# Optimization experiments

Hardware: AMD Instinct MI355X
Metric: run time of the kernel (lower is better)

The kernel has to match this reference:

```python
import jax, jax.numpy as jnp
import numpy as np

N, E, G = 50000, 400000, 64
IN_C, HID, OUT_C, HEADS = 256, 128, 256, 4
LRELU_SLOPE = 0.2
LN_EPS = 1e-5


def setup_inputs() -> dict:
    key = jax.random.key(0)
    ks = jax.random.split(key, 16)
    d = {}
    d["x"] = jax.random.normal(ks[0], (N, IN_C), dtype=jnp.float32)
    d["edge_index"] = jax.random.randint(ks[1], (2, E), 0, N, dtype=jnp.int32)
    d["batch"] = jnp.sort(jax.random.randint(ks[2], (N,), 0, G, dtype=jnp.int32))
    s1 = 1.0 / np.sqrt(IN_C)
    d["W1"] = jax.random.uniform(ks[3], (IN_C, HEADS * HID), jnp.float32, -s1, s1)
    d["att_src1"] = jax.random.normal(ks[4], (HEADS, HID), jnp.float32) * 0.1
    d["att_dst1"] = jax.random.normal(ks[5], (HEADS, HID), jnp.float32) * 0.1
    d["b1"] = jnp.zeros((HEADS * HID,), jnp.float32)
    d["ln1_g"] = jnp.ones((HEADS * HID,), jnp.float32)
    d["ln1_b"] = jnp.zeros((HEADS * HID,), jnp.float32)
    s2 = 1.0 / np.sqrt(HEADS * HID)
    d["W2"] = jax.random.uniform(ks[6], (HEADS * HID, OUT_C), jnp.float32, -s2, s2)
    d["att_src2"] = jax.random.normal(ks[7], (1, OUT_C), jnp.float32) * 0.1
    d["att_dst2"] = jax.random.normal(ks[8], (1, OUT_C), jnp.float32) * 0.1
    d["b2"] = jnp.zeros((OUT_C,), jnp.float32)
    d["ln2_g"] = jnp.ones((OUT_C,), jnp.float32)
    d["ln2_b"] = jnp.zeros((OUT_C,), jnp.float32)
    return d


def _layernorm(x, g, b):
    mu = jnp.mean(x, axis=-1, keepdims=True)
    var = jnp.mean(jnp.square(x - mu), axis=-1, keepdims=True)
    return (x - mu) * jax.lax.rsqrt(var + LN_EPS) * g + b


def _gat_conv(x, src, dst, W, a_src, a_dst, bias):
    # PyG GATConv (eval mode, dropout inactive), self-loops already in src/dst.
    H, C = a_src.shape
    h = (x @ W).reshape(N, H, C)                       # [N,H,C]
    e_src = jnp.einsum('nhc,hc->nh', h, a_src)          # [N,H]
    e_dst = jnp.einsum('nhc,hc->nh', h, a_dst)
    e = jax.nn.leaky_relu(e_src[src] + e_dst[dst], LRELU_SLOPE)  # [Etot,H]
    m = jax.ops.segment_max(e, dst, num_segments=N)     # segment softmax over incoming edges
    ex = jnp.exp(e - m[dst])
    s = jax.ops.segment_sum(ex, dst, num_segments=N)
    alpha = ex / (s[dst] + 1e-16)                       # [Etot,H]
    msg = h[src] * alpha[:, :, None]                    # [Etot,H,C]
    out = jax.ops.segment_sum(msg, dst, num_segments=N) # [N,H,C]
    return out.reshape(N, H * C) + bias


def reference(x, edge_index, batch, W1, att_src1, att_dst1, b1, ln1_g, ln1_b,
              W2, att_src2, att_dst2, b2, ln2_g, ln2_b):
    loops = jnp.arange(N, dtype=edge_index.dtype)
    src = jnp.concatenate([edge_index[0], loops])
    dst = jnp.concatenate([edge_index[1], loops])
    h = _gat_conv(x, src, dst, W1, att_src1, att_dst1, b1)
    h = _layernorm(h, ln1_g, ln1_b)
    h = jax.nn.relu(h)                                  # dropout is identity in eval
    h = _gat_conv(h, src, dst, W2, att_src2, att_dst2, b2)
    h = _layernorm(h, ln2_g, ln2_b)
    # global_mean_pool over graphs
    sums = jax.ops.segment_sum(h, batch, num_segments=G)
    cnts = jax.ops.segment_sum(jnp.ones((N,), h.dtype), batch, num_segments=G)
    return sums / jnp.maximum(cnts, 1.0)[:, None]
```

## Files before the change

kernel.cpp:

```cpp
#include <hip/hip_runtime.h>
#include <hip/hip_bf16.h>
#include <cstdint>

#define LRELU_SLOPE 0.2f

typedef short bf16x8 __attribute__((ext_vector_type(8)));
typedef float f32x4  __attribute__((ext_vector_type(4)));

__device__ __forceinline__ float b2f(unsigned short u) {
  return __uint_as_float(((unsigned int)u) << 16);
}
__device__ __forceinline__ unsigned short f2b(float f) {
  unsigned int u = __float_as_uint(f);
  return (unsigned short)((u + 0x7fff + ((u >> 16) & 1)) >> 16);
}

__device__ __forceinline__ void gload16(const void* g, void* l) {
  __builtin_amdgcn_global_load_lds(
      (const __attribute__((address_space(1))) unsigned int*)g,
      (__attribute__((address_space(3))) unsigned int*)l, 16, 0, 0);
}

__global__ __launch_bounds__(256)
void prep_x_count(const float* __restrict__ x, unsigned short* __restrict__ o,
                  int M, int Mpad, const int* __restrict__ ei, int E, int Etot,
                  int* __restrict__ count) {
  const int i = blockIdx.x * 256 + threadIdx.x;
  if (i < Mpad * 64) {
    const int row = i >> 6;
    const int c4  = (i & 63) * 4;
    ushort4 v = make_ushort4(0, 0, 0, 0);
    if (row < M) {
      const float4 f = *(const float4*)&x[(size_t)row * 256 + c4];
      v = make_ushort4(f2b(f.x), f2b(f.y), f2b(f.z), f2b(f.w));
    }
    *(ushort4*)&o[(size_t)row * 256 + c4] = v;
  }
  if (i < Etot) {
    const int d = (i < E) ? ei[E + i] : (i - E);
    atomicAdd(&count[d], 1);
  }
}

__global__ __launch_bounds__(256)
void cvt_wts(const float* __restrict__ W1, const float* __restrict__ W2,
             unsigned short* __restrict__ W1T, unsigned short* __restrict__ W2T) {
  int j = blockIdx.x * 256 + threadIdx.x;
  if (j < 512 * 256) {
    const int n = j >> 8, k = j & 255;
    W1T[j] = f2b(W1[(size_t)k * 512 + n]);
  } else {
    j -= 512 * 256;
    const int n = j >> 9, k = j & 511;
    W2T[j] = f2b(W2[(size_t)k * 256 + n]);
  }
}

__global__ __launch_bounds__(256)
void scan_blocksum(const int* __restrict__ count, int* __restrict__ bsum, int Nn) {
  const int i0 = blockIdx.x * 1024 + threadIdx.x * 4;
  int s = 0;
#pragma unroll
  for (int k = 0; k < 4; ++k) { const int i = i0 + k; if (i < Nn) s += count[i]; }
#pragma unroll
  for (int off = 1; off < 64; off <<= 1) s += __shfl_xor(s, off);
  __shared__ int ws[4];
  if ((threadIdx.x & 63) == 0) ws[threadIdx.x >> 6] = s;
  __syncthreads();
  if (threadIdx.x == 0) bsum[blockIdx.x] = ws[0] + ws[1] + ws[2] + ws[3];
}

__global__ __launch_bounds__(64)
void scan_top(const int* __restrict__ bsum, int* __restrict__ boff,
              int* __restrict__ rowptrN, int nb) {
  const int t = threadIdx.x;
  const int v = (t < nb) ? bsum[t] : 0;
  int incl = v;
#pragma unroll
  for (int off = 1; off < 64; off <<= 1) {
    const int u = __shfl_up(incl, off);
    if (t >= off) incl += u;
  }
  if (t < nb) boff[t] = incl - v;
  if (t == 63) *rowptrN = incl;
}

__global__ __launch_bounds__(256)
void scan_apply(const int* __restrict__ count, const int* __restrict__ boff,
                int* __restrict__ rowptr, int* __restrict__ cursor, int Nn) {
  const int t = threadIdx.x;
  const int lane = t & 63;
  const int w = t >> 6;
  const int i0 = blockIdx.x * 1024 + t * 4;
  int c[4]; int s = 0;
#pragma unroll
  for (int k = 0; k < 4; ++k) { const int i = i0 + k; c[k] = (i < Nn) ? count[i] : 0; s += c[k]; }
  int incl = s;
#pragma unroll
  for (int off = 1; off < 64; off <<= 1) {
    const int u = __shfl_up(incl, off);
    if (lane >= off) incl += u;
  }
  __shared__ int ws[4];
  if (lane == 63) ws[w] = incl;
  __syncthreads();
  int woff = 0;
  for (int k = 0; k < w; ++k) woff += ws[k];
  int base = boff[blockIdx.x] + woff + incl - s;
#pragma unroll
  for (int k = 0; k < 4; ++k) {
    const int i = i0 + k;
    if (i < Nn) { rowptr[i] = base; cursor[i] = base; base += c[k]; }
  }
}

__global__ __launch_bounds__(256)
void csr_scatter(const int* __restrict__ ei, int E, int Etot,
                 int* __restrict__ cursor, int* __restrict__ srcs,
                 int* __restrict__ dsts) {
  const int i = blockIdx.x * 256 + threadIdx.x;
  if (i >= Etot) return;
  const int s = (i < E) ? ei[i]     : (i - E);
  const int d = (i < E) ? ei[E + i] : (i - E);
  const int pos = atomicAdd(&cursor[d], 1);
  srcs[pos] = s;
  dsts[pos] = d;
}

template<int KSTEPS>
__global__ __launch_bounds__(256)
void gemm_bf16(const unsigned short* __restrict__ A,
               const unsigned short* __restrict__ BT,
               unsigned short* __restrict__ C, int M, int Nn, int K,
               const float* __restrict__ asrc, const float* __restrict__ adst,
               float* __restrict__ es, float* __restrict__ ed,
               int H, int lgC, int esPart) {
  __shared__ __align__(16) unsigned short smA[2][64 * 32];
  __shared__ __align__(16) unsigned short smB[2][128 * 32];
  const int tid  = threadIdx.x;
  const int lane = tid & 63;
  const int wid  = tid >> 6;
  const int wm = wid >> 1, wn = wid & 1;
  const int brow = blockIdx.y * 64;
  const int bcol = blockIdx.x * 128;
  const int u = lane >> 4, r15 = lane & 15;
  const int arow = tid >> 2, aslot = tid & 3;
  const size_t aBase = (size_t)(brow + arow) * K + (aslot ^ (arow & 3)) * 8;
  const int ldsA = arow * 32 + aslot * 8;
  const int brow0 = tid >> 2,        bslot0 = tid & 3;
  const int brow1 = (256 + tid) >> 2, bslot1 = tid & 3;
  const size_t bBase0 = (size_t)(bcol + brow0) * K + (bslot0 ^ (brow0 & 3)) * 8;
  const size_t bBase1 = (size_t)(bcol + brow1) * K + (bslot1 ^ (brow1 & 3)) * 8;
  const int ldsB0 = brow0 * 32 + bslot0 * 8;
  const int ldsB1 = brow1 * 32 + bslot1 * 8;

  auto stage = [&](int buf, int ks) {
    const int k0 = ks * 32;
    gload16(A + aBase + k0, &smA[buf][ldsA]);
    gload16(BT + bBase0 + k0, &smB[buf][ldsB0]);
    gload16(BT + bBase1 + k0, &smB[buf][ldsB1]);
  };

  f32x4 acc[2][4] = {};
  const int sw = u ^ (r15 & 3);

  stage(0, 0);
  asm volatile("s_waitcnt vmcnt(0)" ::: "memory");
  __syncthreads();
  int cur = 0;
#pragma unroll
  for (int ks = 0; ks < KSTEPS; ++ks) {
    if (ks + 1 < KSTEPS) stage(cur ^ 1, ks + 1);
    bf16x8 af[2], bfv[4];
#pragma unroll
    for (int m = 0; m < 2; ++m) {
      const int row = wm * 32 + m * 16 + r15;
      af[m] = *(const bf16x8*)&smA[cur][row * 32 + sw * 8];
    }
#pragma unroll
    for (int n = 0; n < 4; ++n) {
      const int col = wn * 64 + n * 16 + r15;
      bfv[n] = *(const bf16x8*)&smB[cur][col * 32 + sw * 8];
    }
#pragma unroll
    for (int m = 0; m < 2; ++m)
#pragma unroll
      for (int n = 0; n < 4; ++n)
        acc[m][n] = __builtin_amdgcn_mfma_f32_16x16x32_bf16(
            af[m], bfv[n], acc[m][n], 0, 0, 0);
    if (ks + 1 < KSTEPS) {
      asm volatile("s_waitcnt vmcnt(0)" ::: "memory");
      __syncthreads();
      cur ^= 1;
    }
  }

  __syncthreads();
  unsigned short* cb = &smB[0][0];
#pragma unroll
  for (int m = 0; m < 2; ++m)
#pragma unroll
    for (int n = 0; n < 4; ++n) {
      const int col = wn * 64 + n * 16 + r15;
#pragma unroll
      for (int rr = 0; rr < 4; ++rr) {
        const int row = wm * 32 + m * 16 + u * 4 + rr;
        cb[row * 128 + col] = f2b(acc[m][n][rr]);
      }
    }
  __syncthreads();
#pragma unroll
  for (int i = 0; i < 4; ++i) {
    const int idx = (i * 256 + tid) * 8;
    const int row = idx >> 7;
    const int cc  = idx & 127;
    const int grow = brow + row;
    if (grow < M)
      *(float4*)&C[(size_t)grow * Nn + bcol + cc] = *(const float4*)&cb[idx];
  }

  es += (size_t)blockIdx.x * esPart;
  ed += (size_t)blockIdx.x * esPart;
  const int head = bcol >> lgC;
  float asv[4], adv[4];
#pragma unroll
  for (int n = 0; n < 4; ++n) {
    const int cc = bcol + wn * 64 + n * 16 + r15;
    asv[n] = asrc[cc];
    adv[n] = adst[cc];
  }
#pragma unroll
  for (int m = 0; m < 2; ++m) {
#pragma unroll
    for (int rr = 0; rr < 4; ++rr) {
      float pes = 0.f, ped = 0.f;
#pragma unroll
      for (int n = 0; n < 4; ++n) {
        pes = fmaf(acc[m][n][rr], asv[n], pes);
        ped = fmaf(acc[m][n][rr], adv[n], ped);
      }
#pragma unroll
      for (int off = 1; off < 16; off <<= 1) {
        pes += __shfl_xor(pes, off);
        ped += __shfl_xor(ped, off);
      }
      if (r15 == 0) {
        const int row = brow + wm * 32 + m * 16 + u * 4 + rr;
        if (row < M) {
          unsafeAtomicAdd(&es[row * H + head], pes);
          unsafeAtomicAdd(&ed[row * H + head], ped);
        }
      }
    }
  }
}

template<int H>
__global__ __launch_bounds__(256)
void ex_compute(const int* __restrict__ srcs, const int* __restrict__ dsts,
                const float* __restrict__ es, const float* __restrict__ ed,
                float* __restrict__ exCSR, int Etot, int pN) {
  const int p = blockIdx.x * 256 + threadIdx.x;
  if (p >= Etot) return;
  const int sN = srcs[p], dN = dsts[p];
  if constexpr (H == 4) {
    const float4 a = *(const float4*)&es[sN * 4];
    const float4 b = *(const float4*)&ed[dN * 4];
    float e0 = a.x + b.x, e1 = a.y + b.y, e2 = a.z + b.z, e3 = a.w + b.w;
    e0 = (e0 > 0.f) ? e0 : LRELU_SLOPE * e0;
    e1 = (e1 > 0.f) ? e1 : LRELU_SLOPE * e1;
    e2 = (e2 > 0.f) ? e2 : LRELU_SLOPE * e2;
    e3 = (e3 > 0.f) ? e3 : LRELU_SLOPE * e3;
    *(float4*)&exCSR[p * 4] =
        make_float4(__expf(e0), __expf(e1), __expf(e2), __expf(e3));
  } else {
    float e = (es[sN] + es[pN + sN]) + (ed[dN] + ed[pN + dN]);
    e = (e > 0.f) ? e : LRELU_SLOPE * e;
    exCSR[p] = __expf(e);
  }
}

template<int H, int C, bool RELU, bool BFOUT>
__global__ __launch_bounds__(256)
void gat_agg_ln(const int* __restrict__ rowptr, const int* __restrict__ srcs,
                const float* __restrict__ exCSR,
                const unsigned short* __restrict__ h,
                const float* __restrict__ bias, const float* __restrict__ lng,
                const float* __restrict__ lnb, unsigned short* __restrict__ obf,
                float* __restrict__ of32, int Nn) {
  constexpr int HC = H * C;
  constexpr int F  = HC / 64;
  const int wave = threadIdx.x >> 6;
  const int lane = threadIdx.x & 63;
  const int n = blockIdx.x * 4 + wave;
  if (n >= Nn) return;
  const int beg = rowptr[n];
  const int deg = rowptr[n + 1] - beg;
  const int hl = (lane * F) / C;

  float dsum = 0.f;
  if constexpr (H == 4) {
    for (int it = lane; it < deg * 4; it += 64) dsum += exCSR[beg * 4 + it];
#pragma unroll
    for (int off = 4; off < 64; off <<= 1) dsum += __shfl_xor(dsum, off);
    dsum = __shfl(dsum, hl);
  } else {
    for (int it = lane; it < deg; it += 64) dsum += exCSR[beg + it];
#pragma unroll
    for (int off = 1; off < 64; off <<= 1) dsum += __shfl_xor(dsum, off);
  }
  const float inv_s = 1.0f / (dsum + 1e-16f);

  float acc[F];
#pragma unroll
  for (int i = 0; i < F; ++i) acc[i] = 0.f;

  auto fma_rows = [&](const ushort4* v0, const ushort4* v1, const float* a, int cnt) {
    for (int q = 0; q < cnt; ++q) {
      acc[0] = fmaf(b2f(v0[q].x), a[q], acc[0]);
      acc[1] = fmaf(b2f(v0[q].y), a[q], acc[1]);
      acc[2] = fmaf(b2f(v0[q].z), a[q], acc[2]);
      acc[3] = fmaf(b2f(v0[q].w), a[q], acc[3]);
      if constexpr (F == 8) {
        acc[4] = fmaf(b2f(v1[q].x), a[q], acc[4]);
        acc[5] = fmaf(b2f(v1[q].y), a[q], acc[5]);
        acc[6] = fmaf(b2f(v1[q].z), a[q], acc[6]);
        acc[7] = fmaf(b2f(v1[q].w), a[q], acc[7]);
      }
    }
  };

  int j = 0;
  for (; j + 4 <= deg; j += 4) {
    int s4[4];
    float a4[4];
#pragma unroll
    for (int q = 0; q < 4; ++q) s4[q] = srcs[beg + j + q];
#pragma unroll
    for (int q = 0; q < 4; ++q) a4[q] = exCSR[(beg + j + q) * H + hl] * inv_s;
    ushort4 v0[4], v1[4];
#pragma unroll
    for (int q = 0; q < 4; ++q) {
      const unsigned short* hp = &h[(size_t)s4[q] * HC + lane * F];
      v0[q] = *(const ushort4*)hp;
      if constexpr (F == 8) v1[q] = *(const ushort4*)(hp + 4);
    }
    fma_rows(v0, v1, a4, 4);
  }
  for (; j < deg; ++j) {
    const int src = srcs[beg + j];
    const float a = exCSR[(beg + j) * H + hl] * inv_s;
    const unsigned short* hp = &h[(size_t)src * HC + lane * F];
    ushort4 v0 = *(const ushort4*)hp, v1;
    if constexpr (F == 8) v1 = *(const ushort4*)(hp + 4);
    fma_rows(&v0, &v1, &a, 1);
  }

#pragma unroll
  for (int i = 0; i < F; i += 4) {
    const float4 bb = *(const float4*)&bias[lane * F + i];
    acc[i + 0] += bb.x; acc[i + 1] += bb.y;
    acc[i + 2] += bb.z; acc[i + 3] += bb.w;
  }
  float sum = 0.f, sq = 0.f;
#pragma unroll
  for (int i = 0; i < F; ++i) { sum += acc[i]; sq += acc[i] * acc[i]; }
#pragma unroll
  for (int off = 1; off < 64; off <<= 1) {
    sum += __shfl_xor(sum, off);
    sq  += __shfl_xor(sq, off);
  }
  const float mu  = sum / HC;
  const float var = sq / HC - mu * mu;
  const float r   = rsqrtf(var + 1e-5f);
  float y[F];
#pragma unroll
  for (int i = 0; i < F; i += 4) {
    const float4 gg = *(const float4*)&lng[lane * F + i];
    const float4 bl = *(const float4*)&lnb[lane * F + i];
    y[i + 0] = (acc[i + 0] - mu) * r * gg.x + bl.x;
    y[i + 1] = (acc[i + 1] - mu) * r * gg.y + bl.y;
    y[i + 2] = (acc[i + 2] - mu) * r * gg.z + bl.z;
    y[i + 3] = (acc[i + 3] - mu) * r * gg.w + bl.w;
  }
  if constexpr (RELU) {
#pragma unroll
    for (int i = 0; i < F; ++i) y[i] = fmaxf(y[i], 0.f);
  }
  if constexpr (BFOUT) {
    unsigned short* op = &obf[(size_t)n * HC + lane * F];
    *(ushort4*)op = make_ushort4(f2b(y[0]), f2b(y[1]), f2b(y[2]), f2b(y[3]));
    if constexpr (F == 8)
      *(ushort4*)(op + 4) = make_ushort4(f2b(y[4]), f2b(y[5]), f2b(y[6]), f2b(y[7]));
  } else {
    float* op = &of32[(size_t)n * HC + lane * F];
    *(float4*)op = make_float4(y[0], y[1], y[2], y[3]);
    if constexpr (F == 8)
      *(float4*)(op + 4) = make_float4(y[4], y[5], y[6], y[7]);
  }
}

__global__ __launch_bounds__(256)
void pool_partial(const unsigned short* __restrict__ x, const int* __restrict__ batch,
                  float* __restrict__ tmp, int* __restrict__ cnt, int Nn) {
  const int r0 = blockIdx.x * 64;
  const int rend = min(r0 + 64, Nn);
  const int t = threadIdx.x;
  float acc = 0.f;
  int cur = batch[r0];
  int seglen = 0;
  for (int r = r0; r < rend; ++r) {
    const int g = batch[r];
    if (g != cur) {
      unsafeAtomicAdd(&tmp[cur * 256 + t], acc);
      if (t == 0) atomicAdd(&cnt[cur], seglen);
      acc = 0.f; seglen = 0; cur = g;
    }
    acc += b2f(x[(size_t)r * 256 + t]);
    ++seglen;
  }
  unsafeAtomicAdd(&tmp[cur * 256 + t], acc);
  if (t == 0) atomicAdd(&cnt[cur], seglen);
}

__global__ __launch_bounds__(256)
void pool_final(const float* __restrict__ tmp, const int* __restrict__ cnt,
                float* __restrict__ out) {
  const int g = blockIdx.x;
  const int t = threadIdx.x;
  out[g * 256 + t] = tmp[g * 256 + t] / fmaxf((float)cnt[g], 1.f);
}

extern "C" void kernel_launch(void* const* d_in, const int* in_sizes, int n_in,
                              void* d_out, int out_size, void* d_ws, size_t ws_size,
                              hipStream_t stream) {
  const float* x    = (const float*)d_in[0];
  const int*   ei   = (const int*)d_in[1];
  const int*   batch= (const int*)d_in[2];
  const float* W1   = (const float*)d_in[3];
  const float* as1  = (const float*)d_in[4];
  const float* ad1  = (const float*)d_in[5];
  const float* b1   = (const float*)d_in[6];
  const float* g1   = (const float*)d_in[7];
  const float* be1  = (const float*)d_in[8];
  const float* W2   = (const float*)d_in[9];
  const float* as2  = (const float*)d_in[10];
  const float* ad2  = (const float*)d_in[11];
  const float* b2   = (const float*)d_in[12];
  const float* g2   = (const float*)d_in[13];
  const float* be2  = (const float*)d_in[14];

  const int N    = in_sizes[0] / 256;
  const int E    = in_sizes[1] / 2;
  const int Etot = E + N;
  const int Mpad = ((N + 63) / 64) * 64;
  const int NB   = (N + 1023) / 1024;

  float* ws = (float*)d_ws;
  unsigned short* out2 = (unsigned short*)ws;
  unsigned short* A2bf = out2 + (size_t)N * 256;
  unsigned short* A1bf = A2bf;
  unsigned short* h1bf = A2bf + (size_t)Mpad * 512;
  unsigned short* W1T  = h1bf + (size_t)N * 512;
  unsigned short* W2T  = W1T + 512 * 256;
  float* es1 = (float*)(W2T + 512 * 256);
  float* ed1 = es1 + (size_t)N * 4;
  float* es2 = ed1 + (size_t)N * 4;
  float* ed2 = es2 + (size_t)N * 2;
  int* count  = (int*)(ed2 + (size_t)N * 2);
  int* rowptr = count + N;
  int* cursor = rowptr + N + 4;
  int* srcs   = cursor + N;
  int* dsts   = srcs + Etot;
  float* exCSR = (float*)(dsts + Etot);
  float* ptmp = exCSR + (size_t)Etot * 4;
  int*   pcnt = (int*)(ptmp + 64 * 256);
  int*   bsum = pcnt + 64;
  int*   boff = bsum + 64;
  unsigned short* h2bf = h1bf;

  const int eb = (Etot + 255) / 256;

  hipMemsetAsync(es1, 0, (size_t)N * 13 * 4, stream);
  hipMemsetAsync(ptmp, 0, (size_t)(64 * 256 + 64) * 4, stream);
  hipMemsetAsync(A2bf + (size_t)N * 512, 0, (size_t)(Mpad - N) * 512 * 2, stream);

  prep_x_count<<<(Mpad * 64 + 255) / 256, 256, 0, stream>>>(
      x, A1bf, N, Mpad, ei, E, Etot, count);
  cvt_wts<<<(2 * 512 * 256 + 255) / 256, 256, 0, stream>>>(W1, W2, W1T, W2T);

  scan_blocksum<<<NB, 256, 0, stream>>>(count, bsum, N);
  scan_top<<<1, 64, 0, stream>>>(bsum, boff, &rowptr[N], NB);
  scan_apply<<<NB, 256, 0, stream>>>(count, boff, rowptr, cursor, N);
  csr_scatter<<<eb, 256, 0, stream>>>(ei, E, Etot, cursor, srcs, dsts);

  gemm_bf16<8><<<dim3(4, Mpad / 64), 256, 0, stream>>>(
      A1bf, W1T, h1bf, N, 512, 256, as1, ad1, es1, ed1, 4, 7, 0);
  ex_compute<4><<<eb, 256, 0, stream>>>(srcs, dsts, es1, ed1, exCSR, Etot, 0);
  gat_agg_ln<4, 128, true, true><<<(N + 3) / 4, 256, 0, stream>>>(
      rowptr, srcs, exCSR, h1bf, b1, g1, be1, A2bf, nullptr, N);

  gemm_bf16<16><<<dim3(2, Mpad / 64), 256, 0, stream>>>(
      A2bf, W2T, h2bf, N, 256, 512, as2, ad2, es2, ed2, 1, 8, N);
  ex_compute<1><<<eb, 256, 0, stream>>>(srcs, dsts, es2, ed2, exCSR, Etot, N);
  gat_agg_ln<1, 256, false, true><<<(N + 3) / 4, 256, 0, stream>>>(
      rowptr, srcs, exCSR, h2bf, b2, g2, be2, out2, nullptr, N);

  pool_partial<<<(N + 63) / 64, 256, 0, stream>>>(out2, batch, ptmp, pcnt, N);
  pool_final<<<64, 256, 0, stream>>>(ptmp, pcnt, (float*)d_out);
}
```

Before: 319.2 us.

## Shrink GEMM N-tile to 64, unroll aggregation by 8 with packed bf16 loads

The GEMM block tile goes from 64x128 to 64x64, which doubles the grid and halves LDS and accumulator usage. Layer 2 therefore splits its attention-score partials across four column blocks, and both the es/ed buffers and the memset grow to match. The aggregation kernel now gathers 8 neighbor rows at a time using wide uint4/uint2 loads and unpacks bf16 pairs with bit ops, to expose more memory-level parallelism. The smaller tile reloads the A operand more often and adds more atomic adds for the attention scores.

```diff
diff --git a/kernel.cpp b/kernel.cpp
--- a/kernel.cpp
+++ b/kernel.cpp
@@ -135,33 +135,27 @@
                const float* __restrict__ asrc, const float* __restrict__ adst,
                float* __restrict__ es, float* __restrict__ ed,
                int H, int lgC, int esPart) {
-  __shared__ __align__(16) unsigned short smA[2][64 * 32];
-  __shared__ __align__(16) unsigned short smB[2][128 * 32];
+  __shared__ __align__(16) unsigned short sm[2][4096];
   const int tid  = threadIdx.x;
   const int lane = tid & 63;
   const int wid  = tid >> 6;
   const int wm = wid >> 1, wn = wid & 1;
   const int brow = blockIdx.y * 64;
-  const int bcol = blockIdx.x * 128;
+  const int bcol = blockIdx.x * 64;
   const int u = lane >> 4, r15 = lane & 15;
-  const int arow = tid >> 2, aslot = tid & 3;
-  const size_t aBase = (size_t)(brow + arow) * K + (aslot ^ (arow & 3)) * 8;
-  const int ldsA = arow * 32 + aslot * 8;
-  const int brow0 = tid >> 2,        bslot0 = tid & 3;
-  const int brow1 = (256 + tid) >> 2, bslot1 = tid & 3;
-  const size_t bBase0 = (size_t)(bcol + brow0) * K + (bslot0 ^ (brow0 & 3)) * 8;
-  const size_t bBase1 = (size_t)(bcol + brow1) * K + (bslot1 ^ (brow1 & 3)) * 8;
-  const int ldsB0 = brow0 * 32 + bslot0 * 8;
-  const int ldsB1 = brow1 * 32 + bslot1 * 8;
+  const int srow = tid >> 2, sslot = tid & 3;
+  const int sswz = sslot ^ (srow & 3);
+  const size_t aBase = (size_t)(brow + srow) * K + sswz * 8;
+  const size_t bBase = (size_t)(bcol + srow) * K + sswz * 8;
+  const int ldsOff = srow * 32 + sslot * 8;
 
   auto stage = [&](int buf, int ks) {
     const int k0 = ks * 32;
-    gload16(A + aBase + k0, &smA[buf][ldsA]);
-    gload16(BT + bBase0 + k0, &smB[buf][ldsB0]);
-    gload16(BT + bBase1 + k0, &smB[buf][ldsB1]);
+    gload16(A + aBase + k0, &sm[buf][ldsOff]);
+    gload16(BT + bBase + k0, &sm[buf][2048 + ldsOff]);
   };
 
-  f32x4 acc[2][4] = {};
+  f32x4 acc[2][2] = {};
   const int sw = u ^ (r15 & 3);
 
   stage(0, 0);
@@ -171,21 +165,21 @@
 #pragma unroll
   for (int ks = 0; ks < KSTEPS; ++ks) {
     if (ks + 1 < KSTEPS) stage(cur ^ 1, ks + 1);
-    bf16x8 af[2], bfv[4];
+    bf16x8 af[2], bfv[2];
 #pragma unroll
     for (int m = 0; m < 2; ++m) {
       const int row = wm * 32 + m * 16 + r15;
-      af[m] = *(const bf16x8*)&smA[cur][row * 32 + sw * 8];
-    }
-#pragma unroll
-    for (int n = 0; n < 4; ++n) {
-      const int col = wn * 64 + n * 16 + r15;
-      bfv[n] = *(const bf16x8*)&smB[cur][col * 32 + sw * 8];
+      af[m] = *(const bf16x8*)&sm[cur][row * 32 + sw * 8];
+    }
+#pragma unroll
+    for (int n = 0; n < 2; ++n) {
+      const int col = wn * 32 + n * 16 + r15;
+      bfv[n] = *(const bf16x8*)&sm[cur][2048 + col * 32 + sw * 8];
     }
 #pragma unroll
     for (int m = 0; m < 2; ++m)
 #pragma unroll
-      for (int n = 0; n < 4; ++n)
+      for (int n = 0; n < 2; ++n)
         acc[m][n] = __builtin_amdgcn_mfma_f32_16x16x32_bf16(
             af[m], bfv[n], acc[m][n], 0, 0, 0);
     if (ks + 1 < KSTEPS) {
@@ -196,24 +190,24 @@
   }
 
   __syncthreads();
-  unsigned short* cb = &smB[0][0];
+  unsigned short* cb = &sm[0][0];
 #pragma unroll
   for (int m = 0; m < 2; ++m)
 #pragma unroll
-    for (int n = 0; n < 4; ++n) {
-      const int col = wn * 64 + n * 16 + r15;
+    for (int n = 0; n < 2; ++n) {
+      const int col = wn * 32 + n * 16 + r15;
 #pragma unroll
       for (int rr = 0; rr < 4; ++rr) {
         const int row = wm * 32 + m * 16 + u * 4 + rr;
-        cb[row * 128 + col] = f2b(acc[m][n][rr]);
+        cb[row * 64 + col] = f2b(acc[m][n][rr]);
       }
     }
   __syncthreads();
 #pragma unroll
-  for (int i = 0; i < 4; ++i) {
+  for (int i = 0; i < 2; ++i) {
     const int idx = (i * 256 + tid) * 8;
-    const int row = idx >> 7;
-    const int cc  = idx & 127;
+    const int row = idx >> 6;
+    const int cc  = idx & 63;
     const int grow = brow + row;
     if (grow < M)
       *(float4*)&C[(size_t)grow * Nn + bcol + cc] = *(const float4*)&cb[idx];
@@ -222,10 +216,10 @@
   es += (size_t)blockIdx.x * esPart;
   ed += (size_t)blockIdx.x * esPart;
   const int head = bcol >> lgC;
-  float asv[4], adv[4];
-#pragma unroll
-  for (int n = 0; n < 4; ++n) {
-    const int cc = bcol + wn * 64 + n * 16 + r15;
+  float asv[2], adv[2];
+#pragma unroll
+  for (int n = 0; n < 2; ++n) {
+    const int cc = bcol + wn * 32 + n * 16 + r15;
     asv[n] = asrc[cc];
     adv[n] = adst[cc];
   }
@@ -235,7 +229,7 @@
     for (int rr = 0; rr < 4; ++rr) {
       float pes = 0.f, ped = 0.f;
 #pragma unroll
-      for (int n = 0; n < 4; ++n) {
+      for (int n = 0; n < 2; ++n) {
         pes = fmaf(acc[m][n][rr], asv[n], pes);
         ped = fmaf(acc[m][n][rr], adv[n], ped);
       }
@@ -274,7 +268,10 @@
     *(float4*)&exCSR[p * 4] =
         make_float4(__expf(e0), __expf(e1), __expf(e2), __expf(e3));
   } else {
-    float e = (es[sN] + es[pN + sN]) + (ed[dN] + ed[pN + dN]);
+    float se = 0.f, de = 0.f;
+#pragma unroll
+    for (int q = 0; q < 4; ++q) { se += es[q * pN + sN]; de += ed[q * pN + dN]; }
+    float e = se + de;
     e = (e > 0.f) ? e : LRELU_SLOPE * e;
     exCSR[p] = __expf(e);
   }
@@ -315,45 +312,57 @@
 #pragma unroll
   for (int i = 0; i < F; ++i) acc[i] = 0.f;
 
-  auto fma_rows = [&](const ushort4* v0, const ushort4* v1, const float* a, int cnt) {
-    for (int q = 0; q < cnt; ++q) {
-      acc[0] = fmaf(b2f(v0[q].x), a[q], acc[0]);
-      acc[1] = fmaf(b2f(v0[q].y), a[q], acc[1]);
-      acc[2] = fmaf(b2f(v0[q].z), a[q], acc[2]);
-      acc[3] = fmaf(b2f(v0[q].w), a[q], acc[3]);
-      if constexpr (F == 8) {
-        acc[4] = fmaf(b2f(v1[q].x), a[q], acc[4]);
-        acc[5] = fmaf(b2f(v1[q].y), a[q], acc[5]);
-        acc[6] = fmaf(b2f(v1[q].z), a[q], acc[6]);
-        acc[7] = fmaf(b2f(v1[q].w), a[q], acc[7]);
+  auto fma_pack = [&](unsigned int w, float a, int i) {
+    acc[i]     = fmaf(__uint_as_float(w << 16), a, acc[i]);
+    acc[i + 1] = fmaf(__uint_as_float(w & 0xffff0000u), a, acc[i + 1]);
+  };
+
+  int j = 0;
+  for (; j + 8 <= deg; j += 8) {
+    int s8[8];
+#pragma unroll
+    for (int q = 0; q < 8; ++q) s8[q] = srcs[beg + j + q];
+    if constexpr (F == 8) {
+      uint4 g[8];
+#pragma unroll
+      for (int q = 0; q < 8; ++q)
+        g[q] = *(const uint4*)&h[(size_t)s8[q] * HC + lane * 8];
+      float a8[8];
+#pragma unroll
+      for (int q = 0; q < 8; ++q) a8[q] = exCSR[(beg + j + q) * H + hl] * inv_s;
+#pragma unroll
+      for (int q = 0; q < 8; ++q) {
+        fma_pack(g[q].x, a8[q], 0);
+        fma_pack(g[q].y, a8[q], 2);
+        fma_pack(g[q].z, a8[q], 4);
+        fma_pack(g[q].w, a8[q], 6);
       }
-    }
-  };
-
-  int j = 0;
-  for (; j + 4 <= deg; j += 4) {
-    int s4[4];
-    float a4[4];
-#pragma unroll
-    for (int q = 0; q < 4; ++q) s4[q] = srcs[beg + j + q];
-#pragma unroll
-    for (int q = 0; q < 4; ++q) a4[q] = exCSR[(beg + j + q) * H + hl] * inv_s;
-    ushort4 v0[4], v1[4];
-#pragma unroll
-    for (int q = 0; q < 4; ++q) {
-      const unsigned short* hp = &h[(size_t)s4[q] * HC + lane * F];
-      v0[q] = *(const ushort4*)hp;
-      if constexpr (F == 8) v1[q] = *(const ushort4*)(hp + 4);
-    }
-    fma_rows(v0, v1, a4, 4);
+    } else {
+      uint2 g[8];
+#pragma unroll
+      for (int q = 0; q < 8; ++q)
+        g[q] = *(const uint2*)&h[(size_t)s8[q] * HC + lane * 4];
+      float a8[8];
+#pragma unroll
+      for (int q = 0; q < 8; ++q) a8[q] = exCSR[(beg + j + q) * H + hl] * inv_s;
+#pragma unroll
+      for (int q = 0; q < 8; ++q) {
+        fma_pack(g[q].x, a8[q], 0);
+        fma_pack(g[q].y, a8[q], 2);
+      }
+    }
   }
   for (; j < deg; ++j) {
     const int src = srcs[beg + j];
     const float a = exCSR[(beg + j) * H + hl] * inv_s;
-    const unsigned short* hp = &h[(size_t)src * HC + lane * F];
-    ushort4 v0 = *(const ushort4*)hp, v1;
-    if constexpr (F == 8) v1 = *(const ushort4*)(hp + 4);
-    fma_rows(&v0, &v1, &a, 1);
+    if constexpr (F == 8) {
+      const uint4 g = *(const uint4*)&h[(size_t)src * HC + lane * 8];
+      fma_pack(g.x, a, 0); fma_pack(g.y, a, 2);
+      fma_pack(g.z, a, 4); fma_pack(g.w, a, 6);
+    } else {
+      const uint2 g = *(const uint2*)&h[(size_t)src * HC + lane * 4];
+      fma_pack(g.x, a, 0); fma_pack(g.y, a, 2);
+    }
   }
 
 #pragma unroll
@@ -466,8 +475,8 @@
   float* es1 = (float*)(W2T + 512 * 256);
   float* ed1 = es1 + (size_t)N * 4;
   float* es2 = ed1 + (size_t)N * 4;
-  float* ed2 = es2 + (size_t)N * 2;
-  int* count  = (int*)(ed2 + (size_t)N * 2);
+  float* ed2 = es2 + (size_t)N * 4;
+  int* count  = (int*)(ed2 + (size_t)N * 4);
   int* rowptr = count + N;
   int* cursor = rowptr + N + 4;
   int* srcs   = cursor + N;
@@ -481,7 +490,7 @@
 
   const int eb = (Etot + 255) / 256;
 
-  hipMemsetAsync(es1, 0, (size_t)N * 13 * 4, stream);
+  hipMemsetAsync(es1, 0, (size_t)N * 17 * 4, stream);
   hipMemsetAsync(ptmp, 0, (size_t)(64 * 256 + 64) * 4, stream);
   hipMemsetAsync(A2bf + (size_t)N * 512, 0, (size_t)(Mpad - N) * 512 * 2, stream);
 
@@ -494,13 +503,13 @@
   scan_apply<<<NB, 256, 0, stream>>>(count, boff, rowptr, cursor, N);
   csr_scatter<<<eb, 256, 0, stream>>>(ei, E, Etot, cursor, srcs, dsts);
 
-  gemm_bf16<8><<<dim3(4, Mpad / 64), 256, 0, stream>>>(
+  gemm_bf16<8><<<dim3(8, Mpad / 64), 256, 0, stream>>>(
       A1bf, W1T, h1bf, N, 512, 256, as1, ad1, es1, ed1, 4, 7, 0);
   ex_compute<4><<<eb, 256, 0, stream>>>(srcs, dsts, es1, ed1, exCSR, Etot, 0);
   gat_agg_ln<4, 128, true, true><<<(N + 3) / 4, 256, 0, stream>>>(
       rowptr, srcs, exCSR, h1bf, b1, g1, be1, A2bf, nullptr, N);
 
-  gemm_bf16<16><<<dim3(2, Mpad / 64), 256, 0, stream>>>(
+  gemm_bf16<16><<<dim3(4, Mpad / 64), 256, 0, stream>>>(
       A2bf, W2T, h2bf, N, 256, 512, as2, ad2, es2, ed2, 1, 8, N);
   ex_compute<1><<<eb, 256, 0, stream>>>(srcs, dsts, es2, ed2, exCSR, Etot, N);
   gat_agg_ln<1, 256, false, true><<<(N + 3) / 4, 256, 0, stream>>>(
```

New measurement: 393.0 us. 1.23x slower.
